# Kernel tuning notes

Hardware: AMD Instinct MI355X
Metric: run time of the kernel (lower is better)

Reference implementation:

```python
import jax, jax.numpy as jnp
import numpy as np

B, T, D_IN, D_OUT = 4, 2048, 4096, 16384
MAX_INT = 127   # 2**(8-1) - 1
MIN_INT = -128  # -2**(8-1)
THRESH = 0.5
EPS = 1e-8


def setup_inputs() -> dict:
    key = jax.random.key(0)
    kx, kw, kb = jax.random.split(key, 3)
    x = jax.random.normal(kx, (B, T, D_IN), dtype=jnp.float32)
    # kaiming_uniform_(a=sqrt(5)) -> uniform(-1/sqrt(fan_in), 1/sqrt(fan_in))
    bound = 1.0 / np.sqrt(D_IN)
    weight = jax.random.uniform(kw, (D_OUT, D_IN), minval=-bound, maxval=bound, dtype=jnp.float32)
    bias = jax.random.uniform(kb, (D_OUT,), minval=-bound, maxval=bound, dtype=jnp.float32)
    return {"x": x, "weight": weight, "bias": bias}


def reference(x, weight, bias):
    # Per-token 8-bit absmax activation quantization (simulated)
    scale = jnp.max(jnp.abs(x), axis=-1, keepdims=True) / MAX_INT  # (B,T,1)
    x_int = jnp.clip(jnp.round(x / (scale + EPS)), MIN_INT, MAX_INT)
    x_q = x_int * scale
    # Ternary absmean weight quantization with STE
    w_scale = jnp.mean(jnp.abs(weight))
    w_scaled = weight / (w_scale + EPS)
    W_q = jnp.sign(w_scaled) * (jnp.abs(w_scaled) > THRESH).astype(weight.dtype)
    W_ste = weight + jax.lax.stop_gradient(W_q - weight)
    # Dense GEMM on dequantized values: (B,T,D_in) x (D_out,D_in)^T
    return jnp.einsum('btd,od->bto', x_q, W_ste) + bias
```

## Files before the change

kernel.cpp:

```cpp
#include <hip/hip_runtime.h>
#include <stdint.h>

#define B_DIM 4
#define T_DIM 2048
#define D_IN  4096
#define D_OUT 16384
#define M_DIM (B_DIM * T_DIM)
#define NW    ((size_t)D_OUT * (size_t)D_IN)

typedef __attribute__((ext_vector_type(4))) int v4i;

__global__ __launch_bounds__(256) void act_quant_kernel(
    const float* __restrict__ x, int8_t* __restrict__ xq,
    float* __restrict__ scales) {
  const int row = blockIdx.x;
  const float4* xr = (const float4*)(x + (size_t)row * D_IN);
  float4 v[4];
  float amax = 0.f;
#pragma unroll
  for (int c = 0; c < 4; ++c) {
    v[c] = xr[c * 256 + threadIdx.x];
    amax = fmaxf(amax, fmaxf(fmaxf(fabsf(v[c].x), fabsf(v[c].y)),
                             fmaxf(fabsf(v[c].z), fabsf(v[c].w))));
  }
#pragma unroll
  for (int off = 32; off > 0; off >>= 1)
    amax = fmaxf(amax, __shfl_down(amax, off, 64));
  __shared__ float smax[4];
  const int lane = threadIdx.x & 63, wave = threadIdx.x >> 6;
  if (lane == 0) smax[wave] = amax;
  __syncthreads();
  amax = fmaxf(fmaxf(smax[0], smax[1]), fmaxf(smax[2], smax[3]));
  const float scale = amax * (1.0f / 127.0f);
  const float denom = scale + 1e-8f;
  if (threadIdx.x == 0) scales[row] = scale;
  int* outp = (int*)(xq + (size_t)row * D_IN);
#pragma unroll
  for (int c = 0; c < 4; ++c) {
    int q0 = min(127, max(-128, __float2int_rn(v[c].x / denom)));
    int q1 = min(127, max(-128, __float2int_rn(v[c].y / denom)));
    int q2 = min(127, max(-128, __float2int_rn(v[c].z / denom)));
    int q3 = min(127, max(-128, __float2int_rn(v[c].w / denom)));
    outp[c * 256 + threadIdx.x] =
        (q0 & 255) | ((q1 & 255) << 8) | ((q2 & 255) << 16) | ((q3 & 255) << 24);
  }
}

__global__ __launch_bounds__(256) void wabs_kernel(const float* __restrict__ w,
                                                   double* __restrict__ out) {
  const float4* w4 = (const float4*)w;
  const size_t n4 = NW / 4;
  double acc = 0.0;
  for (size_t i = (size_t)blockIdx.x * blockDim.x + threadIdx.x; i < n4;
       i += (size_t)gridDim.x * blockDim.x) {
    float4 v = w4[i];
    acc += (double)fabsf(v.x) + (double)fabsf(v.y);
    acc += (double)fabsf(v.z) + (double)fabsf(v.w);
  }
#pragma unroll
  for (int off = 32; off > 0; off >>= 1) acc += __shfl_down(acc, off, 64);
  __shared__ double ssum[4];
  const int lane = threadIdx.x & 63, wave = threadIdx.x >> 6;
  if (lane == 0) ssum[wave] = acc;
  __syncthreads();
  if (threadIdx.x == 0) atomicAdd(out, ssum[0] + ssum[1] + ssum[2] + ssum[3]);
}

__global__ __launch_bounds__(256) void wquant_kernel(
    const float* __restrict__ w, const double* __restrict__ sumAbs,
    int8_t* __restrict__ wq) {
  const float ws = (float)(*sumAbs / (double)NW) + 1e-8f;
  const float4* w4 = (const float4*)w;
  int* outp = (int*)wq;
  const size_t stride = (size_t)gridDim.x * blockDim.x;
  size_t i = (size_t)blockIdx.x * blockDim.x + threadIdx.x;
#pragma unroll
  for (int c = 0; c < 4; ++c, i += stride) {
    float4 v = w4[i];
    float t0 = v.x / ws, t1 = v.y / ws, t2 = v.z / ws, t3 = v.w / ws;
    int q0 = (fabsf(t0) > 0.5f) ? ((t0 > 0.f) ? 1 : -1) : 0;
    int q1 = (fabsf(t1) > 0.5f) ? ((t1 > 0.f) ? 1 : -1) : 0;
    int q2 = (fabsf(t2) > 0.5f) ? ((t2 > 0.f) ? 1 : -1) : 0;
    int q3 = (fabsf(t3) > 0.5f) ? ((t3 > 0.f) ? 1 : -1) : 0;
    outp[i] = (q0 & 255) | ((q1 & 255) << 8) | ((q2 & 255) << 16) | ((q3 & 255) << 24);
  }
}

#define BM 128
#define BN 128
#define BK 64
#define KTILES (D_IN / BK)

__global__ __launch_bounds__(256) void gemm_i8_kernel(
    const int8_t* __restrict__ xq, const int8_t* __restrict__ wq,
    const float* __restrict__ scales, const float* __restrict__ bias,
    float* __restrict__ out) {
  __shared__ __align__(16) int8_t lA[BM * BK];
  __shared__ __align__(16) int8_t lB[BN * BK];

  const int tid = threadIdx.x;
  const int lane = tid & 63;
  const int wave = tid >> 6;
  const int wr = wave >> 1;
  const int wc = wave & 1;
  const int quad = lane >> 4;
  const int r16 = lane & 15;

  const int bm = blockIdx.y * BM;
  const int bn = blockIdx.x * BN;

  const int srow = tid >> 2;
  const int schunk = (tid & 3) ^ ((tid >> 3) & 3);
  const int8_t* gA = xq + (size_t)bm * D_IN;
  const int8_t* gB = wq + (size_t)bn * D_IN;

  const int fp = (quad ^ ((r16 >> 1) & 3)) * 16;

  v4i acc[4][4] = {};

  for (int kt = 0; kt < KTILES; ++kt) {
    const int k0 = kt * BK;
    __syncthreads();
#pragma unroll
    for (int i = 0; i < 2; ++i) {
      const int rl = i * 64 + srow;
      const size_t goff = (size_t)rl * D_IN + k0 + schunk * 16;
      __builtin_amdgcn_global_load_lds(
          (const __attribute__((address_space(1))) void*)(gA + goff),
          (__attribute__((address_space(3))) void*)(lA + i * 4096 + tid * 16),
          16, 0, 0);
      __builtin_amdgcn_global_load_lds(
          (const __attribute__((address_space(1))) void*)(gB + goff),
          (__attribute__((address_space(3))) void*)(lB + i * 4096 + tid * 16),
          16, 0, 0);
    }
    __syncthreads();

    v4i af[4], bf[4];
#pragma unroll
    for (int i = 0; i < 4; ++i) {
      const int m = wr * 64 + i * 16 + r16;
      af[i] = *(const v4i*)(lA + m * 64 + fp);
      const int n = wc * 64 + i * 16 + r16;
      bf[i] = *(const v4i*)(lB + n * 64 + fp);
    }
#pragma unroll
    for (int i = 0; i < 4; ++i)
#pragma unroll
      for (int j = 0; j < 4; ++j)
        acc[i][j] = __builtin_amdgcn_mfma_i32_16x16x64_i8(af[i], bf[j],
                                                          acc[i][j], 0, 0, 0);
  }

  float bs[4];
#pragma unroll
  for (int j = 0; j < 4; ++j) bs[j] = bias[bn + wc * 64 + j * 16 + r16];

#pragma unroll
  for (int i = 0; i < 4; ++i) {
#pragma unroll
    for (int reg = 0; reg < 4; ++reg) {
      const int m = bm + wr * 64 + i * 16 + quad * 4 + reg;
      const float s = scales[m];
      float* orow = out + (size_t)m * D_OUT + bn + wc * 64 + r16;
#pragma unroll
      for (int j = 0; j < 4; ++j) {
        orow[j * 16] = (float)acc[i][j][reg] * s + bs[j];
      }
    }
  }
}

extern "C" void kernel_launch(void* const* d_in, const int* in_sizes, int n_in,
                              void* d_out, int out_size, void* d_ws,
                              size_t ws_size, hipStream_t stream) {
  const float* x = (const float*)d_in[0];
  const float* w = (const float*)d_in[1];
  const float* bias = (const float*)d_in[2];
  float* out = (float*)d_out;

  char* ws = (char*)d_ws;
  double* d_sum = (double*)ws;
  float* d_scales = (float*)(ws + 256);
  int8_t* d_xq = (int8_t*)(ws + 33024);
  int8_t* d_wq = (int8_t*)(ws + 33024 + (size_t)M_DIM * D_IN);

  hipMemsetAsync(d_sum, 0, sizeof(double), stream);

  act_quant_kernel<<<M_DIM, 256, 0, stream>>>(x, d_xq, d_scales);
  wabs_kernel<<<2048, 256, 0, stream>>>(w, d_sum);
  wquant_kernel<<<16384, 256, 0, stream>>>(w, d_sum, d_wq);
  gemm_i8_kernel<<<dim3(D_OUT / BN, M_DIM / BM), 256, 0, stream>>>(
      d_xq, d_wq, d_scales, bias, out);
}
```

Before: 1.412 ms.

## Rewrite int8 GEMM with 256x256 tiles, double-buffered LDS and interleaved prefetch

Replaces the single-buffered 128x128x64 int8 MFMA GEMM with a 256x256x128 tile on 512 threads. Two LDS buffers hold A and B, and global-to-LDS loads for the next K tiles are interleaved with MFMA phases under fine-grained barriers, vmcnt waits and setprio. It also adds an XOR-swizzled LDS layout and a block-index swizzle for L2 locality. The aim is to hide load latency and raise arithmetic intensity, at the cost of 128KB of LDS, higher register pressure and a fragile hand-tuned wait schedule.

```diff
diff --git a/kernel.cpp b/kernel.cpp
--- a/kernel.cpp
+++ b/kernel.cpp
@@ -86,81 +86,151 @@
   }
 }
 
-#define BM 128
-#define BN 128
-#define BK 64
-#define KTILES (D_IN / BK)
-
-__global__ __launch_bounds__(256) void gemm_i8_kernel(
+#define BM 256
+#define BN 256
+#define BKB 128
+#define NKT (D_IN / BKB)
+#define A0s 0
+#define B0s 32768
+#define A1s 65536
+#define B1s 98304
+
+#define BARRIER() __builtin_amdgcn_s_barrier()
+#define VMWAIT(n) asm volatile("s_waitcnt vmcnt(" #n ")" ::: "memory")
+#define LGKM0()   asm volatile("s_waitcnt lgkmcnt(0)" ::: "memory")
+
+__global__ __launch_bounds__(512, 2) void gemm_i8_kernel(
     const int8_t* __restrict__ xq, const int8_t* __restrict__ wq,
     const float* __restrict__ scales, const float* __restrict__ bias,
     float* __restrict__ out) {
-  __shared__ __align__(16) int8_t lA[BM * BK];
-  __shared__ __align__(16) int8_t lB[BN * BK];
+  __shared__ __align__(16) int8_t lds[131072];
 
   const int tid = threadIdx.x;
   const int lane = tid & 63;
   const int wave = tid >> 6;
-  const int wr = wave >> 1;
-  const int wc = wave & 1;
+  const int wr = wave >> 2;
+  const int wc = wave & 3;
   const int quad = lane >> 4;
   const int r16 = lane & 15;
 
-  const int bm = blockIdx.y * BM;
-  const int bn = blockIdx.x * BN;
-
-  const int srow = tid >> 2;
-  const int schunk = (tid & 3) ^ ((tid >> 3) & 3);
-  const int8_t* gA = xq + (size_t)bm * D_IN;
-  const int8_t* gB = wq + (size_t)bn * D_IN;
-
-  const int fp = (quad ^ ((r16 >> 1) & 3)) * 16;
-
-  v4i acc[4][4] = {};
-
-  for (int kt = 0; kt < KTILES; ++kt) {
-    const int k0 = kt * BK;
-    __syncthreads();
-#pragma unroll
-    for (int i = 0; i < 2; ++i) {
-      const int rl = i * 64 + srow;
-      const size_t goff = (size_t)rl * D_IN + k0 + schunk * 16;
-      __builtin_amdgcn_global_load_lds(
-          (const __attribute__((address_space(1))) void*)(gA + goff),
-          (__attribute__((address_space(3))) void*)(lA + i * 4096 + tid * 16),
-          16, 0, 0);
-      __builtin_amdgcn_global_load_lds(
-          (const __attribute__((address_space(1))) void*)(gB + goff),
-          (__attribute__((address_space(3))) void*)(lB + i * 4096 + tid * 16),
-          16, 0, 0);
-    }
-    __syncthreads();
-
-    v4i af[4], bf[4];
-#pragma unroll
-    for (int i = 0; i < 4; ++i) {
-      const int m = wr * 64 + i * 16 + r16;
-      af[i] = *(const v4i*)(lA + m * 64 + fp);
-      const int n = wc * 64 + i * 16 + r16;
-      bf[i] = *(const v4i*)(lB + n * 64 + fp);
-    }
-#pragma unroll
-    for (int i = 0; i < 4; ++i)
-#pragma unroll
-      for (int j = 0; j < 4; ++j)
-        acc[i][j] = __builtin_amdgcn_mfma_i32_16x16x64_i8(af[i], bf[j],
-                                                          acc[i][j], 0, 0, 0);
-  }
+  const int bid = blockIdx.x;
+  const int swz = (bid & 7) * 256 + (bid >> 3);
+  const int bm = (swz >> 6) * BM;
+  const int bn = (swz & 63) * BN;
+
+  const int sr = tid >> 3;
+  const int scol = ((tid & 7) << 4) ^ ((sr & 7) << 4);
+  const int8_t* gA = xq + (size_t)(bm + sr) * D_IN + scol;
+  const int8_t* gB = wq + (size_t)(bn + sr) * D_IN + scol;
+
+#define STAGE(opbase, gp, q, kt)                                          \
+  __builtin_amdgcn_global_load_lds(                                       \
+      (const __attribute__((address_space(1))) void*)((gp) +              \
+          (size_t)(q) * (64 * D_IN) + (kt) * BKB),                        \
+      (__attribute__((address_space(3))) void*)(lds + (opbase) +          \
+          (q) * 8192 + tid * 16),                                         \
+      16, 0, 0);
+
+  const int sw = (r16 & 7) << 4;
+  int koff[2];
+  koff[0] = (quad * 16) ^ sw;
+  koff[1] = (quad * 16 + 64) ^ sw;
+  const int arow = wr * 128 + r16;
+  const int brow = wc * 64 + r16;
+
+  v4i acc[8][4] = {};
+  v4i a[4][2], b[4][2];
+
+#define LDA(base, h)                                                      \
+  _Pragma("unroll") for (int i = 0; i < 4; ++i) {                         \
+    _Pragma("unroll") for (int kk = 0; kk < 2; ++kk)                      \
+        a[i][kk] = *(const v4i*)&lds[(base) +                             \
+            (arow + (h) * 64 + i * 16) * BKB + koff[kk]];                 \
+  }
+#define LDB(base, j0)                                                     \
+  _Pragma("unroll") for (int j = 0; j < 2; ++j) {                         \
+    _Pragma("unroll") for (int kk = 0; kk < 2; ++kk)                      \
+        b[(j0) + j][kk] = *(const v4i*)&lds[(base) +                      \
+            (brow + ((j0) + j) * 16) * BKB + koff[kk]];                   \
+  }
+#define MM(h, j0)                                                         \
+  LGKM0();                                                                \
+  __builtin_amdgcn_s_setprio(1);                                          \
+  _Pragma("unroll") for (int kk = 0; kk < 2; ++kk) {                      \
+    _Pragma("unroll") for (int i = 0; i < 4; ++i) {                       \
+      _Pragma("unroll") for (int j = 0; j < 2; ++j)                       \
+          acc[(h) * 4 + i][(j0) + j] =                                    \
+              __builtin_amdgcn_mfma_i32_16x16x64_i8(                      \
+                  a[i][kk], b[(j0) + j][kk],                              \
+                  acc[(h) * 4 + i][(j0) + j], 0, 0, 0);                   \
+    }                                                                     \
+  }                                                                       \
+  __builtin_amdgcn_s_setprio(0);
+
+  STAGE(A0s, gA, 0, 0) STAGE(A0s, gA, 1, 0) STAGE(A0s, gA, 2, 0) STAGE(A0s, gA, 3, 0)
+  STAGE(B0s, gB, 0, 0) STAGE(B0s, gB, 1, 0) STAGE(B0s, gB, 2, 0) STAGE(B0s, gB, 3, 0)
+  STAGE(A1s, gA, 0, 1) STAGE(A1s, gA, 2, 1)
+  STAGE(B1s, gB, 0, 1) STAGE(B1s, gB, 1, 1) STAGE(B1s, gB, 2, 1) STAGE(B1s, gB, 3, 1)
+  VMWAIT(6);
+  BARRIER();
+
+#pragma unroll 1
+  for (int t = 0; t < NKT / 2; ++t) {
+    const int kt1 = 2 * t + 1;
+    const int kt2 = (2 * t + 2) & (NKT - 1);
+    const int kt3 = (2 * t + 3) & (NKT - 1);
+    LDA(A0s, 0) LDB(B0s, 0)
+    STAGE(A1s, gA, 1, kt1) STAGE(A1s, gA, 3, kt1)
+    BARRIER();
+    MM(0, 0)
+    BARRIER();
+    LDB(B0s, 2)
+    STAGE(A0s, gA, 0, kt2) STAGE(A0s, gA, 2, kt2)
+    BARRIER();
+    MM(0, 2)
+    BARRIER();
+    LDA(A0s, 1)
+    STAGE(B0s, gB, 0, kt2) STAGE(B0s, gB, 1, kt2)
+    BARRIER();
+    MM(1, 2)
+    BARRIER();
+    STAGE(B0s, gB, 2, kt2) STAGE(B0s, gB, 3, kt2)
+    BARRIER();
+    MM(1, 0)
+    VMWAIT(6);
+    BARRIER();
+    LDA(A1s, 0) LDB(B1s, 0)
+    STAGE(A0s, gA, 1, kt2) STAGE(A0s, gA, 3, kt2)
+    BARRIER();
+    MM(0, 0)
+    BARRIER();
+    LDB(B1s, 2)
+    STAGE(A1s, gA, 0, kt3) STAGE(A1s, gA, 2, kt3)
+    BARRIER();
+    MM(0, 2)
+    BARRIER();
+    LDA(A1s, 1)
+    STAGE(B1s, gB, 0, kt3) STAGE(B1s, gB, 1, kt3)
+    BARRIER();
+    MM(1, 2)
+    BARRIER();
+    STAGE(B1s, gB, 2, kt3) STAGE(B1s, gB, 3, kt3)
+    BARRIER();
+    MM(1, 0)
+    VMWAIT(6);
+    BARRIER();
+  }
+  VMWAIT(0);
 
   float bs[4];
 #pragma unroll
   for (int j = 0; j < 4; ++j) bs[j] = bias[bn + wc * 64 + j * 16 + r16];
 
 #pragma unroll
-  for (int i = 0; i < 4; ++i) {
+  for (int i = 0; i < 8; ++i) {
 #pragma unroll
     for (int reg = 0; reg < 4; ++reg) {
-      const int m = bm + wr * 64 + i * 16 + quad * 4 + reg;
+      const int m = bm + wr * 128 + i * 16 + quad * 4 + reg;
       const float s = scales[m];
       float* orow = out + (size_t)m * D_OUT + bn + wc * 64 + r16;
 #pragma unroll
@@ -190,6 +260,5 @@
   act_quant_kernel<<<M_DIM, 256, 0, stream>>>(x, d_xq, d_scales);
   wabs_kernel<<<2048, 256, 0, stream>>>(w, d_sum);
   wquant_kernel<<<16384, 256, 0, stream>>>(w, d_sum, d_wq);
-  gemm_i8_kernel<<<dim3(D_OUT / BN, M_DIM / BM), 256, 0, stream>>>(
-      d_xq, d_wq, d_scales, bias, out);
-}
+  gemm_i8_kernel<<<2048, 512, 0, stream>>>(d_xq, d_wq, d_scales, bias, out);
+}
```

Result: faster. 1.250 ms (-11.5%).
